# Performance work log

Measured on AMD Instinct MI355X. Metric: run time of the kernel, lower is better.

Reference implementation:

```python
import jax, jax.numpy as jnp
import numpy as np

MODEL_DIM = 128
WINDOW = 512
KERNEL = 512
N_BANDS = 128
N_ATOMS = 16
N_SAMPLES = 2 ** 15
STEP = WINDOW // 2
N_FRAMES = N_SAMPLES // STEP  # 128
N_HEADS = 4
D_FF = MODEL_DIM
N_LAYERS = 6
N_FREQS = 16
POS_CH = 2 * N_FREQS + 1  # 33
SR = 22050.0


def mel_filterbank():
    # Mel scale from 40 Hz to nyquist, gammatone-like: here use morlet-style
    # windowed sinusoids as in zounds FilterBank: for the reference we build
    # N_BANDS bandpass FIR filters of length KERNEL (fixed constants, treated
    # as non-learned buffers).
    nyq = SR / 2.0
    def hz_to_mel(h):
        return 2595.0 * np.log10(1 + h / 700.0)
    def mel_to_hz(m):
        return 700.0 * (10 ** (m / 2595.0) - 1)
    mels = np.linspace(hz_to_mel(40.0), hz_to_mel(nyq), N_BANDS + 2)
    hz = mel_to_hz(mels)
    centers = hz[1:-1]
    bandwidths = (hz[2:] - hz[:-2]) * 0.1
    t = np.arange(KERNEL) / SR
    filters = np.zeros((N_BANDS, KERNEL), dtype=np.float32)
    for i in range(N_BANDS):
        env = np.exp(-0.5 * ((t - t.mean()) * bandwidths[i] * 2 * np.pi) ** 2)
        filters[i] = (np.sin(2 * np.pi * centers[i] * t) * env).astype(np.float32)
    # normalize filters
    norms = np.linalg.norm(filters, axis=-1, keepdims=True) + 1e-8
    filters = filters / norms
    return jnp.asarray(filters)


def pos_encoded(batch, time, n_freqs):
    # [B, time, 2*n_freqs+1]: linear position plus sin/cos at doubling freqs
    pos = jnp.linspace(-1.0, 1.0, time, dtype=jnp.float32)
    feats = [pos[:, None]]
    for i in range(n_freqs):
        feats.append(jnp.sin((2.0 ** i) * pos * jnp.pi)[:, None])
        feats.append(jnp.cos((2.0 ** i) * pos * jnp.pi)[:, None])
    p = jnp.concatenate(feats, axis=-1)  # [time, 33]
    return jnp.broadcast_to(p[None], (batch, time, p.shape[-1]))


def layer_norm(x, g, b, eps=1e-5):
    mu = jnp.mean(x, axis=-1, keepdims=True)
    var = jnp.var(x, axis=-1, keepdims=True)
    return (x - mu) * jax.lax.rsqrt(var + eps) * g + b


def mha(x, p):
    B, S, D = x.shape
    hd = D // N_HEADS
    qkv = x @ p['w_qkv'].T + p['b_qkv']  # [B,S,3D]
    q, k, v = jnp.split(qkv, 3, axis=-1)
    def heads(t):
        return t.reshape(B, S, N_HEADS, hd).transpose(0, 2, 1, 3)
    q, k, v = heads(q), heads(k), heads(v)
    scores = jnp.einsum('bhqd,bhkd->bhqk', q, k) / jnp.sqrt(jnp.float32(hd))
    attn = jax.nn.softmax(scores, axis=-1)
    o = jnp.einsum('bhqk,bhkd->bhqd', attn, v)
    o = o.transpose(0, 2, 1, 3).reshape(B, S, D)
    return o @ p['w_o'].T + p['b_o']


def encoder_layer(x, p):
    # post-norm (torch default norm_first=False), relu activation
    x = layer_norm(x + mha(x, p), p['ln1_g'], p['ln1_b'])
    h = jax.nn.relu(x @ p['w1'].T + p['b1']) @ p['w2'].T + p['b2']
    x = layer_norm(x + h, p['ln2_g'], p['ln2_b'])
    return x


def transformer(x, layers):
    for p in layers:
        x = encoder_layer(x, p)
    return x


def _mk_layer(key):
    ks = jax.random.split(key, 4)
    s = 0.1
    D = MODEL_DIM
    return {
        'w_qkv': jax.random.uniform(ks[0], (3 * D, D), minval=-s, maxval=s),
        'b_qkv': jnp.zeros((3 * D,)),
        'w_o': jax.random.uniform(ks[1], (D, D), minval=-s, maxval=s),
        'b_o': jnp.zeros((D,)),
        'w1': jax.random.uniform(ks[2], (D_FF, D), minval=-s, maxval=s),
        'b1': jnp.zeros((D_FF,)),
        'w2': jax.random.uniform(ks[3], (D, D_FF), minval=-s, maxval=s),
        'b2': jnp.zeros((D,)),
        'ln1_g': jnp.ones((D,)), 'ln1_b': jnp.zeros((D,)),
        'ln2_g': jnp.ones((D,)), 'ln2_b': jnp.zeros((D,)),
    }


def setup_inputs() -> dict:
    key = jax.random.key(0)
    ks = jax.random.split(key, 20)
    B = 8
    x = jax.random.normal(ks[0], (B, 1, N_SAMPLES), dtype=jnp.float32)
    s = 0.1
    ctx_layers = [_mk_layer(ks[1 + i]) for i in range(N_LAYERS)]
    dec_layers = [_mk_layer(ks[7 + i]) for i in range(N_LAYERS)]
    params = {
        'filters': mel_filterbank(),  # [N_BANDS, KERNEL], fixed buffer
        'embed_w': jax.random.uniform(ks[13], (MODEL_DIM, MODEL_DIM + POS_CH), minval=-s, maxval=s),
        'embed_b': jnp.zeros((MODEL_DIM,)),
        'embed2_w': jax.random.uniform(ks[14], (MODEL_DIM, MODEL_DIM + POS_CH), minval=-s, maxval=s),
        'embed2_b': jnp.zeros((MODEL_DIM,)),
        'env_w': jax.random.uniform(ks[15], (1, MODEL_DIM), minval=-s, maxval=s),
        'env_b': jnp.zeros((1,)),
        'samp_w': jax.random.uniform(ks[16], (WINDOW, MODEL_DIM), minval=-s, maxval=s),
        'samp_b': jnp.zeros((WINDOW,)),
    }
    # flatten layer params into dict entries
    out = {'x': x}
    out.update(params)
    for i, p in enumerate(ctx_layers):
        for k, v in p.items():
            out[f'ctx{i}_{k}'] = v
    for i, p in enumerate(dec_layers):
        for k, v in p.items():
            out[f'dec{i}_{k}'] = v
    return out


LAYER_KEYS = ['w_qkv', 'b_qkv', 'w_o', 'b_o', 'w1', 'b1', 'w2', 'b2',
              'ln1_g', 'ln1_b', 'ln2_g', 'ln2_b']


def _forward(x, filters, embed_w, embed_b, embed2_w, embed2_b,
             env_w, env_b, samp_w, samp_b, ctx_layers, dec_layers):
    B = x.shape[0]
    # filterbank: conv1d with 'same'-ish padding as zounds (padding=KERNEL//2)
    spec = jax.lax.conv_general_dilated(
        x, filters[:, None, :],  # [O=128, I=1, K=512]
        window_strides=(1,), padding=[(KERNEL // 2, KERNEL // 2)],
        dimension_numbers=('NCH', 'OIH', 'NCH'))  # [B,128,~32768]
    # temporal pooling: avg pool window 512 stride 256 over abs
    pooled = jax.lax.reduce_window(
        jnp.abs(spec), 0.0, jax.lax.add,
        window_dimensions=(1, 1, 512), window_strides=(1, 1, 256),
        padding=[(0, 0), (0, 0), (256, 256)]) / 512.0
    n = pooled[..., :N_FRAMES]  # [B,128,128]
    pos = pos_encoded(B, N_FRAMES, N_FREQS).transpose(0, 2, 1)  # [B,33,128]
    n = jnp.concatenate([pos, n], axis=1)  # [B,161,128]
    n = jnp.einsum('oc,bct->bot', embed_w, n) + embed_b[None, :, None]
    n = n.transpose(0, 2, 1)  # [B,T,D]
    h = transformer(n, ctx_layers)  # context
    h = h.transpose(0, 2, 1)  # [B,D,T]
    norms = (jnp.einsum('oc,bct->bot', env_w, h) + env_b[None, :, None]).reshape(B, -1)
    norms = jax.nn.softmax(norms, axis=-1)
    values, indices = jax.lax.top_k(norms, N_ATOMS)  # [B,K]
    # vectorized gather-scale-scatter: n[b,:,idx] = h[b,:,idx]*val
    sel = jnp.take_along_axis(h, indices[:, None, :], axis=2)  # [B,D,K]
    sel = sel * values[:, None, :]
    sparse = jnp.zeros_like(h)
    bidx = jnp.arange(B)[:, None, None]
    didx = jnp.arange(MODEL_DIM)[None, :, None]
    sparse = sparse.at[bidx, didx, indices[:, None, :]].set(sel)
    n = jnp.concatenate([pos, sparse], axis=1)
    n = jnp.einsum('oc,bct->bot', embed2_w, n) + embed2_b[None, :, None]
    n = n.transpose(0, 2, 1)
    n = transformer(n, dec_layers)
    n = n.transpose(0, 2, 1)  # [B,D,T]
    # to_samples: 1x1 conv D->WINDOW then permute -> [B,T,WINDOW]
    n = jnp.einsum('oc,bct->bto', samp_w, n) + samp_b[None, None, :]
    # hamming window
    t = jnp.arange(WINDOW, dtype=jnp.float32)
    ham = 0.54 - 0.46 * jnp.cos(2 * jnp.pi * t / (WINDOW - 1))
    n = n * ham[None, None, :]
    # overlap-add with hop = WINDOW//2
    T = n.shape[1]
    out_len = STEP * (T - 1) + WINDOW
    frame_pos = jnp.arange(T)[:, None] * STEP + jnp.arange(WINDOW)[None, :]
    out = jnp.zeros((B, out_len), dtype=n.dtype)
    out = out.at[:, frame_pos.reshape(-1)].add(n.reshape(B, -1))
    return out[:, None, :N_SAMPLES]


def reference(x, filters, embed_w, embed_b, embed2_w, embed2_b,
              env_w, env_b, samp_w, samp_b, **layer_params):
    ctx_layers = [{k: layer_params[f'ctx{i}_{k}'] for k in LAYER_KEYS}
                  for i in range(N_LAYERS)]
    dec_layers = [{k: layer_params[f'dec{i}_{k}'] for k in LAYER_KEYS}
                  for i in range(N_LAYERS)]
    return _forward(x, filters, embed_w, embed_b, embed2_w, embed2_b,
                    env_w, env_b, samp_w, samp_b, ctx_layers, dec_layers)
```

## Files before the change

### kernel.cpp

```cpp
#include <hip/hip_runtime.h>
#include <math.h>

#define NB 8
#define NS 32768
#define SEQ 128
#define DIM 128
#define KER 512
#define PI_D 3.14159265358979323846

#define ALOAD(p)     __hip_atomic_load((p), __ATOMIC_RELAXED, __HIP_MEMORY_SCOPE_AGENT)
#define ASTORE(p, v) __hip_atomic_store((p), (v), __ATOMIC_RELAXED, __HIP_MEMORY_SCOPE_AGENT)

typedef __attribute__((ext_vector_type(8))) short bfrag;
typedef __attribute__((ext_vector_type(16))) float f32x16;

__global__ void pos_k(float* __restrict__ posT, float* __restrict__ ham) {
    int t = threadIdx.x;
    if (t < 128) {
        double p = (double)((float)(-1.0 + 2.0 * (double)t / 127.0));
        posT[t * 33 + 0] = (float)p;
        for (int i = 0; i < 16; ++i) {
            double a = ldexp(p, i) * PI_D;
            posT[t * 33 + 1 + 2 * i] = (float)sin(a);
            posT[t * 33 + 2 + 2 * i] = (float)cos(a);
// ... 113 lines not shown
        for (int m = 1; m <= 16; m <<= 1) { s0 += __shfl_xor(s0, m); s1 += __shfl_xor(s1, m); }
        if ((lane & 31) == 0) {
            int rowoff = (r & 3) + 8 * (r >> 2) + 4 * g;
            atomicAdd(&Pp[mbase + rowoff], s0);
            atomicAdd(&Pp[mbase + 32 + rowoff], s1);
        }
    }
    __syncthreads();
    if (t < 128) P[((size_t)b * 128 + t) * 128 + c] = Pp[t];
}

struct PackPtrs { const float* p[51]; };

__global__ void pack_k(PackPtrs pp, float4* __restrict__ dst) {
    int m = blockIdx.y;
    const float* src = pp.p[m];
    int N, K, KT; size_t off;
    if (m < 12)      { N = 384; K = 128; KT = 32; off = (size_t)m * 12288; }
    else if (m < 24) { N = 128; K = 128; KT = 32; off = 147456 + (size_t)(m - 12) * 4096; }
    else if (m < 36) { N = 128; K = 128; KT = 32; off = 196608 + (size_t)(m - 24) * 4096; }
    else if (m < 48) { N = 128; K = 128; KT = 32; off = 245760 + (size_t)(m - 36) * 4096; }
    else if (m == 48){ N = 128; K = 161; KT = 41; off = 294912; }
    else if (m == 49){ N = 128; K = 161; KT = 41; off = 300160; }
    else             { N = 512; K = 128; KT = 32; off = 305408; }
    int idx = blockIdx.x * 256 + threadIdx.x;
    int total = (N >> 6) * KT * 64;
    if (idx >= total) return;
    int ln = idx & 63;
    int kt = (idx >> 6) % KT;
    int ct = idx / (KT * 64);
    int cc = ct * 64 + ln;
    int k0 = kt * 4;
    float4 v;
    v.x = (k0 + 0 < K) ? src[(size_t)cc * K + k0 + 0] : 0.f;
    v.y = (k0 + 1 < K) ? src[(size_t)cc * K + k0 + 1] : 0.f;
    v.z = (k0 + 2 < K) ? src[(size_t)cc * K + k0 + 2] : 0.f;
    v.w = (k0 + 3 < K) ? src[(size_t)cc * K + k0 + 3] : 0.f;
    dst[off + idx] = v;
}

struct MegaArgs {
    const float* b_qkv[12]; const float* b_o[12]; const float* b1[12]; const float* b2[12];
    const float* ln1g[12]; const float* ln1b[12]; const float* ln2g[12]; const float* ln2b[12];
    const float* embed_b; const float* embed2_b; const float* env_w; const float* env_b;
    const float* samp_b;
    const float* posT; const float* ham; const float* P;
    const float4* Wp;
    float* KV;
    float* envbuf; float* Y; float* out;
    unsigned* ctr;
};

struct __align__(16) SM {
    float KV[128][129];
    union { float S[16][128]; float partial[16][128]; };
    float Aq[4][128];
    float Ax[4][128];
    float Ax2[4][128];
    float Ah[4][128];
    float cv[4][176];
    float red2[16];
    int   red2i[8];
    float tvals[128], tout[128], Linv[16];
};

__device__ __forceinline__ void gbarb(unsigned* ctr, unsigned& bi) {
    asm volatile("s_waitcnt vmcnt(0)" ::: "memory");
    __syncthreads();
    if (threadIdx.x == 0) {
        bi += 1;
        __hip_atomic_fetch_add(ctr, 1u, __ATOMIC_RELAXED, __HIP_MEMORY_SCOPE_AGENT);
        unsigned target = bi * 32u;
        while (__hip_atomic_load(ctr, __ATOMIC_RELAXED, __HIP_MEMORY_SCOPE_AGENT) < target) {
            __builtin_amdgcn_s_sleep(1);
        }
    }
    __syncthreads();
}

template <int NCB>
__device__ __forceinline__ void gemm_acc(const float* A, int astride, const float4* Wp,
                                         int KT, int t, float (*acc)[4]) {
    int cidx = t & 127, kq = t >> 7;
    int KTq = (KT + 3) >> 2;
    int kt0 = kq * KTq;
    int kt1 = kt0 + KTq; if (kt1 > KT) kt1 = KT;
#pragma unroll
    for (int i = 0; i < NCB; ++i) { acc[i][0] = 0.f; acc[i][1] = 0.f; acc[i][2] = 0.f; acc[i][3] = 0.f; }
    for (int kt = kt0; kt < kt1; ++kt) {
        float4 a0 = *(const float4*)(A + 0 * astride + kt * 4);
        float4 a1 = *(const float4*)(A + 1 * astride + kt * 4);
        float4 a2 = *(const float4*)(A + 2 * astride + kt * 4);
        float4 a3 = *(const float4*)(A + 3 * astride + kt * 4);
#pragma unroll
        for (int i = 0; i < NCB; ++i) {
            int cb = cidx + i * 128;
            float4 w = Wp[((size_t)((cb >> 6) * KT + kt)) * 64 + (cb & 63)];
            acc[i][0] += a0.x * w.x + a0.y * w.y + a0.z * w.z + a0.w * w.w;
            acc[i][1] += a1.x * w.x + a1.y * w.y + a1.z * w.z + a1.w * w.w;
            acc[i][2] += a2.x * w.x + a2.y * w.y + a2.z * w.z + a2.w * w.w;
            acc[i][3] += a3.x * w.x + a3.y * w.y + a3.z * w.z + a3.w * w.w;
        }
    }
}

__device__ __forceinline__ float gemm_reduce(const float* a4, int t, SM& sm) {
    int cidx = t & 127, kq = t >> 7;
    __syncthreads();
#pragma unroll
    for (int r = 0; r < 4; ++r) sm.partial[r * 4 + kq][cidx] = a4[r];
    __syncthreads();
    int rsel = t >> 7;
    return sm.partial[rsel * 4 + 0][cidx] + sm.partial[rsel * 4 + 1][cidx]
         + sm.partial[rsel * 4 + 2][cidx] + sm.partial[rsel * 4 + 3][cidx];
}

__device__ __forceinline__ float lnorm(float v, int t, const float* g, const float* be, SM& sm) {
    float s = v, s2 = v * v;
#pragma unroll
    for (int mm = 1; mm <= 32; mm <<= 1) { s += __shfl_xor(s, mm); s2 += __shfl_xor(s2, mm); }
    int w = t >> 6;
    if ((t & 63) == 0) { sm.red2[w * 2] = s; sm.red2[w * 2 + 1] = s2; }
    __syncthreads();
    int r = t >> 7;
    float S = sm.red2[(2 * r) * 2] + sm.red2[(2 * r + 1) * 2];
    float S2 = sm.red2[(2 * r) * 2 + 1] + sm.red2[(2 * r + 1) * 2 + 1];
    float mu = S * (1.f / 128.f);
    float var = S2 * (1.f / 128.f) - mu * mu;
    float res = (v - mu) * rsqrtf(var + 1e-5f) * g[t & 127] + be[t & 127];
    __syncthreads();
    return res;
}

__device__ __forceinline__ void qkv_tail(const MegaArgs& a, SM& sm, int l, int t, int rowbase) {
    const float4* qkvp = a.Wp + (size_t)l * 12288;
    float acc3[3][4];
    gemm_acc<3>(&sm.Ax[0][0], 128, qkvp, 32, t, acc3);
    int c = t & 127, rs = t >> 7;
    const float* bq = a.b_qkv[l];
    float* KVp = a.KV + (size_t)(l & 1) * 262144;
    float vq = gemm_reduce(acc3[0], t, sm) + bq[c];
    sm.Aq[rs][c] = vq;
    float vk = gemm_reduce(acc3[1], t, sm) + bq[128 + c];
    ASTORE(&KVp[(size_t)(rowbase + rs) * 256 + c], vk);
    float vv = gemm_reduce(acc3[2], t, sm) + bq[256 + c];
    ASTORE(&KVp[(size_t)(rowbase + rs) * 256 + 128 + c], vv);
}

__global__ void __launch_bounds__(512, 1) mega_k(MegaArgs a) {
    __shared__ SM sm;
    const int t = threadIdx.x;
    const int bid = blockIdx.x;
    const int rowbase = bid * 4;
    const int b = rowbase >> 7;
    const int tfr = rowbase & 127;
    const int c = t & 127;
    const int rs = t >> 7;
    unsigned bctr = 0;
    unsigned* myctr = a.ctr + b * 16;

    const float4* embedp  = a.Wp + 294912;
    const float4* embed2p = a.Wp + 300160;
    const float4* sampp   = a.Wp + 305408;

    {
        int tf = tfr + rs;
        for (int j = c; j < 176; j += 128) {
            float val = 0.f;
            if (j < 33) val = a.posT[tf * 33 + j];
            else if (j < 161) {
                int o = j - 33;
                float p1 = a.P[((size_t)(b * 128 + o)) * 128 + tf];
                float p0 = (tf > 0) ? a.P[((size_t)(b * 128 + o)) * 128 + tf - 1] : 0.f;
                val = (p0 + p1) * (1.f / 512.f);
            }
            sm.cv[rs][j] = val;
        }
        __syncthreads();
        float acc1[1][4];
        gemm_acc<1>(&sm.cv[0][0], 176, embedp, 41, t, acc1);
        float v = gemm_reduce(acc1[0], t, sm) + a.embed_b[c];
        sm.Ax[rs][c] = v;
        __syncthreads();
        qkv_tail(a, sm, 0, t, rowbase);
        gbarb(myctr, bctr);
    }

    for (int l = 0; l < 12; ++l) {
        if (l == 6) {
            float v = (t < 128) ? ALOAD(&a.envbuf[b * 128 + t]) : -1e30f;
            float m_ = v;
#pragma unroll
            for (int mm = 1; mm <= 32; mm <<= 1) m_ = fmaxf(m_, __shfl_xor(m_, mm));
            if ((t & 63) == 0) sm.red2[(t >> 6) * 2] = m_;
            __syncthreads();
            float mx = fmaxf(sm.red2[0], sm.red2[2]);
            float e = (t < 128) ? expf(v - mx) : 0.f;
            float ssum = e;
#pragma unroll
            for (int mm = 1; mm <= 32; mm <<= 1) ssum += __shfl_xor(ssum, mm);
            __syncthreads();
            if ((t & 63) == 0) sm.red2[(t >> 6) * 2 + 1] = ssum;
            __syncthreads();
            float lsum = sm.red2[1] + sm.red2[3];
            if (t < 128) { sm.tvals[t] = e / lsum; sm.tout[t] = 0.f; }
            __syncthreads();
            for (int it = 0; it < 16; ++it) {
                float cv_ = (t < 128) ? sm.tvals[t] : -2.f;
                int ci = t & 127;
#pragma unroll
                for (int mm = 1; mm <= 32; mm <<= 1) {
                    float ov = __shfl_xor(cv_, mm);
                    int oi = __shfl_xor(ci, mm);
                    if (ov > cv_ || (ov == cv_ && oi < ci)) { cv_ = ov; ci = oi; }
                }
                if ((t & 63) == 0) { sm.red2[(t >> 6) * 2] = cv_; sm.red2i[t >> 6] = ci; }
                __syncthreads();
                if (t == 0) {
                    float v0 = sm.red2[0], v1 = sm.red2[2];
                    int i0 = sm.red2i[0], i1 = sm.red2i[1];
                    float bv; int bi2;
                    if (v1 > v0 || (v1 == v0 && i1 < i0)) { bv = v1; bi2 = i1; }
                    else { bv = v0; bi2 = i0; }
                    sm.tout[bi2] = bv;
                    sm.tvals[bi2] = -3.f;
                }
                __syncthreads();
            }
            float sclr = sm.tout[tfr + rs];
            for (int j = c; j < 176; j += 128) {
                float val = 0.f;
                if (j < 33) val = a.posT[(tfr + rs) * 33 + j];
                else if (j < 161) val = sm.Ax[rs][j - 33] * sclr;
                sm.cv[rs][j] = val;
            }
            __syncthreads();
            float acc1[1][4];
            gemm_acc<1>(&sm.cv[0][0], 176, embed2p, 41, t, acc1);
            float vv = gemm_reduce(acc1[0], t, sm) + a.embed2_b[c];
            sm.Ax[rs][c] = vv;
            __syncthreads();
            qkv_tail(a, sm, 6, t, rowbase);
            gbarb(myctr, bctr);
        }

        const float4* op  = a.Wp + 147456 + (size_t)l * 4096;
        const float4* w1p = a.Wp + 196608 + (size_t)l * 4096;
        const float4* w2p = a.Wp + 245760 + (size_t)l * 4096;
        const float* KVg = a.KV + (size_t)(l & 1) * 262144 + (size_t)b * 32768;

        {
            float kst[32], vst[32];
#pragma unroll
            for (int j = 0; j < 32; ++j) {
                int f = j * 512 + t;
                kst[j] = ALOAD(&KVg[(size_t)(f >> 7) * 256 + (f & 127)]);
            }
#pragma unroll
            for (int j = 0; j < 32; ++j) {
                int f = j * 512 + t;
                vst[j] = ALOAD(&KVg[(size_t)(f >> 7) * 256 + 128 + (f & 127)]);
            }
            int cd = t & 127, r0 = t >> 7;
#pragma unroll
            for (int j = 0; j < 32; ++j) sm.KV[cd][j * 4 + r0] = kst[j];
            __syncthreads();
            {
                int h = t >> 7, k = c;
                float s0 = 0.f, s1 = 0.f, s2 = 0.f, s3 = 0.f;
#pragma unroll
                for (int d = 0; d < 32; ++d) {
                    float kvv = sm.KV[h * 32 + d][k];
                    s0 += sm.Aq[0][h * 32 + d] * kvv;
                    s1 += sm.Aq[1][h * 32 + d] * kvv;
                    s2 += sm.Aq[2][h * 32 + d] * kvv;
                    s3 += sm.Aq[3][h * 32 + d] * kvv;
                }
                const float scl = 0.17677669529663687f;
                sm.S[h * 4 + 0][k] = s0 * scl;
                sm.S[h * 4 + 1][k] = s1 * scl;
                sm.S[h * 4 + 2][k] = s2 * scl;
                sm.S[h * 4 + 3][k] = s3 * scl;
            }
            __syncthreads();
#pragma unroll
            for (int j = 0; j < 32; ++j) sm.KV[cd][j * 4 + r0] = vst[j];
            {
                int row = t >> 5, l32 = t & 31;
                float v0 = sm.S[row][l32], v1 = sm.S[row][l32 + 32];
                float v2 = sm.S[row][l32 + 64], v3 = sm.S[row][l32 + 96];
                float mx = fmaxf(fmaxf(v0, v1), fmaxf(v2, v3));
#pragma unroll
                for (int mm = 1; mm <= 16; mm <<= 1) mx = fmaxf(mx, __shfl_xor(mx, mm));
                float e0 = __expf(v0 - mx), e1 = __expf(v1 - mx);
                float e2 = __expf(v2 - mx), e3 = __expf(v3 - mx);
                float ls = e0 + e1 + e2 + e3;
#pragma unroll
                for (int mm = 1; mm <= 16; mm <<= 1) ls += __shfl_xor(ls, mm);
                sm.S[row][l32] = e0; sm.S[row][l32 + 32] = e1;
                sm.S[row][l32 + 64] = e2; sm.S[row][l32 + 96] = e3;
                if (l32 == 0) sm.Linv[row] = 1.f / ls;
            }
            __syncthreads();
            {
                int h = t >> 7, r = (t >> 5) & 3, d = t & 31;
                const float* Pr = &sm.S[h * 4 + r][0];
                float o = 0.f;
#pragma unroll 8
                for (int k2 = 0; k2 < 128; ++k2) o += Pr[k2] * sm.KV[h * 32 + d][k2];
                sm.Ah[r][h * 32 + d] = o * sm.Linv[h * 4 + r];
            }
            __syncthreads();
        }
        {
            float acc1[1][4];
            gemm_acc<1>(&sm.Ah[0][0], 128, op, 32, t, acc1);
            float v = gemm_reduce(acc1[0], t, sm);
            v += a.b_o[l][c] + sm.Ax[rs][c];
            v = lnorm(v, t, a.ln1g[l], a.ln1b[l], sm);
            sm.Ax2[rs][c] = v;
            __syncthreads();
        }
        {
            float acc1[1][4];
            gemm_acc<1>(&sm.Ax2[0][0], 128, w1p, 32, t, acc1);
            float v = fmaxf(gemm_reduce(acc1[0], t, sm) + a.b1[l][c], 0.f);
            sm.Ah[rs][c] = v;
            __syncthreads();
            float acc2[1][4];
            gemm_acc<1>(&sm.Ah[0][0], 128, w2p, 32, t, acc2);
            float v2 = gemm_reduce(acc2[0], t, sm) + a.b2[l][c] + sm.Ax2[rs][c];
            v2 = lnorm(v2, t, a.ln2g[l], a.ln2b[l], sm);
            sm.Ax[rs][c] = v2;
            __syncthreads();
        }
        if (l == 5) {
            float pv = sm.Ax[rs][c] * a.env_w[c];
#pragma unroll
            for (int mm = 1; mm <= 32; mm <<= 1) pv += __shfl_xor(pv, mm);
            int w = t >> 6;
            if ((t & 63) == 0) sm.red2[w * 2] = pv;
            __syncthreads();
            if (t < 4) ASTORE(&a.envbuf[rowbase + t],
                              sm.red2[(2 * t) * 2] + sm.red2[(2 * t + 1) * 2] + a.env_b[0]);
            __syncthreads();
        } else if (l == 11) {
            float acc4[4][4];
            gemm_acc<4>(&sm.Ax[0][0], 128, sampp, 32, t, acc4);
#pragma unroll
            for (int i = 0; i < 4; ++i) {
                float v = gemm_reduce(acc4[i], t, sm);
                int cg = c + i * 128;
                v += a.samp_b[cg];
                v *= a.ham[cg];
                ASTORE(&a.Y[((size_t)(rowbase + rs)) * 512 + cg], v);
            }
        } else {
            qkv_tail(a, sm, l + 1, t, rowbase);
        }
        gbarb(myctr, bctr);
    }

    {
        int b32 = bid & 31;
#pragma unroll
        for (int i = 0; i < 2; ++i) {
            int il = b32 * 512 + t + i * 16384;
            int t0 = il >> 8, w0 = il & 255;
            float acc = ALOAD(&a.Y[((size_t)(b * 128 + t0)) * 512 + w0]);
            if (t0 > 0) acc += ALOAD(&a.Y[((size_t)(b * 128 + t0 - 1)) * 512 + w0 + 256]);
            a.out[(size_t)b * 32768 + il] = acc;
        }
    }
}

extern "C" void kernel_launch(void* const* d_in, const int* in_sizes, int n_in,
                              void* d_out, int out_size, void* d_ws, size_t ws_size,
                              hipStream_t stream) {
    const float* x        = (const float*)d_in[0];
    const float* filters  = (const float*)d_in[1];
    const float* embed_w  = (const float*)d_in[2];
    const float* embed_b  = (const float*)d_in[3];
    const float* embed2_w = (const float*)d_in[4];
    const float* embed2_b = (const float*)d_in[5];
    const float* env_w    = (const float*)d_in[6];
    const float* env_b    = (const float*)d_in[7];
    const float* samp_w   = (const float*)d_in[8];
    const float* samp_b   = (const float*)d_in[9];

    float* ws = (float*)d_ws;
    float* P     = ws;
    float* posT  = ws + 131072;
    float* hamw  = ws + 135424;
    float* envb  = ws + 135936;
    float* KV    = ws + 136960;
    float* Y     = ws + 661248;
    float4* Wp   = (float4*)(ws + 1185536);
    unsigned* ctr = (unsigned*)(ws + 2472704);
    unsigned short* xhi = (unsigned short*)Y;
    unsigned short* xlo = (unsigned short*)(Y + 131072);
    unsigned short* Fph = (unsigned short*)KV;
    unsigned short* Fpl = (unsigned short*)(KV + 32768);

    pos_k<<<1, 512, 0, stream>>>(posT, hamw);
    bfsplit_k<<<1024, 256, 0, stream>>>(x, xhi, xlo, NB * NS);
    fpack_k<<<256, 256, 0, stream>>>(filters, Fph, Fpl);
    conv_mfma_k<<<dim3(128, 8), 512, 0, stream>>>(xhi, xlo, Fph, Fpl, P);

    PackPtrs pp;
    for (int l = 0; l < 12; ++l) {
        int base = (l < 6) ? 10 + l * 12 : 82 + (l - 6) * 12;
        pp.p[l]      = (const float*)d_in[base + 0];
        pp.p[12 + l] = (const float*)d_in[base + 2];
        pp.p[24 + l] = (const float*)d_in[base + 4];
        pp.p[36 + l] = (const float*)d_in[base + 6];
    }
    pp.p[48] = embed_w; pp.p[49] = embed2_w; pp.p[50] = samp_w;
    pack_k<<<dim3(64, 51), 256, 0, stream>>>(pp, Wp);

    hipMemsetAsync(ctr, 0, 1024, stream);

    MegaArgs ma;
    for (int l = 0; l < 12; ++l) {
        int base = (l < 6) ? 10 + l * 12 : 82 + (l - 6) * 12;
        ma.b_qkv[l] = (const float*)d_in[base + 1];
        ma.b_o[l]   = (const float*)d_in[base + 3];
        ma.b1[l]    = (const float*)d_in[base + 5];
        ma.b2[l]    = (const float*)d_in[base + 7];
        ma.ln1g[l]  = (const float*)d_in[base + 8];
        ma.ln1b[l]  = (const float*)d_in[base + 9];
        ma.ln2g[l]  = (const float*)d_in[base + 10];
        ma.ln2b[l]  = (const float*)d_in[base + 11];
    }
    ma.embed_b = embed_b; ma.embed2_b = embed2_b;
    ma.env_w = env_w; ma.env_b = env_b; ma.samp_b = samp_b;
    ma.posT = posT; ma.ham = hamw; ma.P = P;
    ma.Wp = (const float4*)Wp;
    ma.KV = KV; ma.envbuf = envb; ma.Y = Y; ma.out = (float*)d_out;
    ma.ctr = ctr;

    mega_k<<<256, 512, 0, stream>>>(ma);
}
```

Before: 348.7 us.

## Split persistent megakernel into 512 half-size blocks with chunked K/V staging

The persistent kernel now runs 512 blocks of 256 threads, each owning 2 sequence rows instead of 4, so per-layer work is spread over twice as many blocks (two per CU). The GEMM helpers reduce over 2 k-slices and write all partial sums with one barrier instead of one pair of barriers per output. Attention stages K and V through shared memory in 64-row halves, prefetching the next half into registers while the current one is used. The aim is more parallelism and fewer barriers per layer. The cost is that every block still reads the full K/V of its batch, which doubles that traffic, and the grid barrier now has to wait for 64 blocks per batch.

```diff
diff --git a/kernel.cpp b/kernel.cpp
--- a/kernel.cpp
+++ b/kernel.cpp
@@ -189,16 +189,16 @@
 };
 
 struct __align__(16) SM {
-    float KV[128][129];
-    union { float S[16][128]; float partial[16][128]; };
-    float Aq[4][128];
-    float Ax[4][128];
-    float Ax2[4][128];
-    float Ah[4][128];
-    float cv[4][176];
+    float KVs[64][129];
+    union { float S[8][128]; float partial[16][128]; };
+    float Aq[2][128];
+    float Ax[2][128];
+    float Ax2[2][128];
+    float Ah[2][128];
+    float cv[2][176];
     float red2[16];
     int   red2i[8];
-    float tvals[128], tout[128], Linv[16];
+    float tvals[128], tout[128], Linv[8];
 };
 
 __device__ __forceinline__ void gbarb(unsigned* ctr, unsigned& bi) {
@@ -207,7 +207,7 @@
     if (threadIdx.x == 0) {
         bi += 1;
         __hip_atomic_fetch_add(ctr, 1u, __ATOMIC_RELAXED, __HIP_MEMORY_SCOPE_AGENT);
-        unsigned target = bi * 32u;
+        unsigned target = bi * 64u;
         while (__hip_atomic_load(ctr, __ATOMIC_RELAXED, __HIP_MEMORY_SCOPE_AGENT) < target) {
             __builtin_amdgcn_s_sleep(1);
         }
@@ -216,40 +216,39 @@
 }
 
 template <int NCB>
-__device__ __forceinline__ void gemm_acc(const float* A, int astride, const float4* Wp,
-                                         int KT, int t, float (*acc)[4]) {
+__device__ __forceinline__ void gemm_acc2(const float* A, int astride, const float4* Wp,
+                                          int KT, int t, float (*acc)[2]) {
     int cidx = t & 127, kq = t >> 7;
-    int KTq = (KT + 3) >> 2;
+    int KTq = (KT + 1) >> 1;
     int kt0 = kq * KTq;
     int kt1 = kt0 + KTq; if (kt1 > KT) kt1 = KT;
 #pragma unroll
-    for (int i = 0; i < NCB; ++i) { acc[i][0] = 0.f; acc[i][1] = 0.f; acc[i][2] = 0.f; acc[i][3] = 0.f; }
+    for (int i = 0; i < NCB; ++i) { acc[i][0] = 0.f; acc[i][1] = 0.f; }
     for (int kt = kt0; kt < kt1; ++kt) {
         float4 a0 = *(const float4*)(A + 0 * astride + kt * 4);
         float4 a1 = *(const float4*)(A + 1 * astride + kt * 4);
-        float4 a2 = *(const float4*)(A + 2 * astride + kt * 4);
-        float4 a3 = *(const float4*)(A + 3 * astride + kt * 4);
 #pragma unroll
         for (int i = 0; i < NCB; ++i) {
             int cb = cidx + i * 128;
             float4 w = Wp[((size_t)((cb >> 6) * KT + kt)) * 64 + (cb & 63)];
             acc[i][0] += a0.x * w.x + a0.y * w.y + a0.z * w.z + a0.w * w.w;
             acc[i][1] += a1.x * w.x + a1.y * w.y + a1.z * w.z + a1.w * w.w;
-            acc[i][2] += a2.x * w.x + a2.y * w.y + a2.z * w.z + a2.w * w.w;
-            acc[i][3] += a3.x * w.x + a3.y * w.y + a3.z * w.z + a3.w * w.w;
-        }
-    }
-}
-
-__device__ __forceinline__ float gemm_reduce(const float* a4, int t, SM& sm) {
-    int cidx = t & 127, kq = t >> 7;
+        }
+    }
+}
+
+template <int NCB>
+__device__ __forceinline__ void gemm_red_write(const float (*acc)[2], int t, SM& sm) {
+    int c = t & 127, kq = t >> 7;
+#pragma unroll
+    for (int i = 0; i < NCB; ++i)
+#pragma unroll
+        for (int r = 0; r < 2; ++r)
+            sm.partial[(i * 2 + r) * 2 + kq][c] = acc[i][r];
     __syncthreads();
-#pragma unroll
-    for (int r = 0; r < 4; ++r) sm.partial[r * 4 + kq][cidx] = a4[r];
-    __syncthreads();
-    int rsel = t >> 7;
-    return sm.partial[rsel * 4 + 0][cidx] + sm.partial[rsel * 4 + 1][cidx]
-         + sm.partial[rsel * 4 + 2][cidx] + sm.partial[rsel * 4 + 3][cidx];
+}
+__device__ __forceinline__ float rdp(SM& sm, int i, int rr, int c) {
+    return sm.partial[(i * 2 + rr) * 2 + 0][c] + sm.partial[(i * 2 + rr) * 2 + 1][c];
 }
 
 __device__ __forceinline__ float lnorm(float v, int t, const float* g, const float* be, SM& sm) {
@@ -271,28 +270,29 @@
 
 __device__ __forceinline__ void qkv_tail(const MegaArgs& a, SM& sm, int l, int t, int rowbase) {
     const float4* qkvp = a.Wp + (size_t)l * 12288;
-    float acc3[3][4];
-    gemm_acc<3>(&sm.Ax[0][0], 128, qkvp, 32, t, acc3);
-    int c = t & 127, rs = t >> 7;
+    float acc3[3][2];
+    gemm_acc2<3>(&sm.Ax[0][0], 128, qkvp, 32, t, acc3);
+    gemm_red_write<3>(acc3, t, sm);
+    int c = t & 127, rr = t >> 7;
     const float* bq = a.b_qkv[l];
     float* KVp = a.KV + (size_t)(l & 1) * 262144;
-    float vq = gemm_reduce(acc3[0], t, sm) + bq[c];
-    sm.Aq[rs][c] = vq;
-    float vk = gemm_reduce(acc3[1], t, sm) + bq[128 + c];
-    ASTORE(&KVp[(size_t)(rowbase + rs) * 256 + c], vk);
-    float vv = gemm_reduce(acc3[2], t, sm) + bq[256 + c];
-    ASTORE(&KVp[(size_t)(rowbase + rs) * 256 + 128 + c], vv);
-}
-
-__global__ void __launch_bounds__(512, 1) mega_k(MegaArgs a) {
+    float vq = rdp(sm, 0, rr, c) + bq[c];
+    sm.Aq[rr][c] = vq;
+    float vk = rdp(sm, 1, rr, c) + bq[128 + c];
+    ASTORE(&KVp[(size_t)(rowbase + rr) * 256 + c], vk);
+    float vv = rdp(sm, 2, rr, c) + bq[256 + c];
+    ASTORE(&KVp[(size_t)(rowbase + rr) * 256 + 128 + c], vv);
+}
+
+__global__ void __launch_bounds__(256, 2) mega_k(MegaArgs a) {
     __shared__ SM sm;
     const int t = threadIdx.x;
     const int bid = blockIdx.x;
-    const int rowbase = bid * 4;
+    const int rowbase = bid * 2;
     const int b = rowbase >> 7;
     const int tfr = rowbase & 127;
     const int c = t & 127;
-    const int rs = t >> 7;
+    const int rr = t >> 7;
     unsigned bctr = 0;
     unsigned* myctr = a.ctr + b * 16;
 
@@ -301,7 +301,7 @@
     const float4* sampp   = a.Wp + 305408;
 
     {
-        int tf = tfr + rs;
+        int tf = tfr + rr;
         for (int j = c; j < 176; j += 128) {
             float val = 0.f;
             if (j < 33) val = a.posT[tf * 33 + j];
@@ -311,13 +311,14 @@
                 float p0 = (tf > 0) ? a.P[((size_t)(b * 128 + o)) * 128 + tf - 1] : 0.f;
                 val = (p0 + p1) * (1.f / 512.f);
             }
-            sm.cv[rs][j] = val;
+            sm.cv[rr][j] = val;
         }
         __syncthreads();
-        float acc1[1][4];
-        gemm_acc<1>(&sm.cv[0][0], 176, embedp, 41, t, acc1);
-        float v = gemm_reduce(acc1[0], t, sm) + a.embed_b[c];
-        sm.Ax[rs][c] = v;
+        float acc1[1][2];
+        gemm_acc2<1>(&sm.cv[0][0], 176, embedp, 41, t, acc1);
+        gemm_red_write<1>(acc1, t, sm);
+        float v = rdp(sm, 0, rr, c) + a.embed_b[c];
+        sm.Ax[rr][c] = v;
         __syncthreads();
         qkv_tail(a, sm, 0, t, rowbase);
         gbarb(myctr, bctr);
@@ -364,18 +365,19 @@
                 }
                 __syncthreads();
             }
-            float sclr = sm.tout[tfr + rs];
+            float sclr = sm.tout[tfr + rr];
             for (int j = c; j < 176; j += 128) {
                 float val = 0.f;
-                if (j < 33) val = a.posT[(tfr + rs) * 33 + j];
-                else if (j < 161) val = sm.Ax[rs][j - 33] * sclr;
-                sm.cv[rs][j] = val;
-            }
-            __syncthreads();
-            float acc1[1][4];
-            gemm_acc<1>(&sm.cv[0][0], 176, embed2p, 41, t, acc1);
-            float vv = gemm_reduce(acc1[0], t, sm) + a.embed2_b[c];
-            sm.Ax[rs][c] = vv;
+                if (j < 33) val = a.posT[(tfr + rr) * 33 + j];
+                else if (j < 161) val = sm.Ax[rr][j - 33] * sclr;
+                sm.cv[rr][j] = val;
+            }
+            __syncthreads();
+            float acc1[1][2];
+            gemm_acc2<1>(&sm.cv[0][0], 176, embed2p, 41, t, acc1);
+            gemm_red_write<1>(acc1, t, sm);
+            float vv = rdp(sm, 0, rr, c) + a.embed2_b[c];
+            sm.Ax[rr][c] = vv;
             __syncthreads();
             qkv_tail(a, sm, 6, t, rowbase);
             gbarb(myctr, bctr);
@@ -387,41 +389,52 @@
         const float* KVg = a.KV + (size_t)(l & 1) * 262144 + (size_t)b * 32768;
 
         {
-            float kst[32], vst[32];
-#pragma unroll
-            for (int j = 0; j < 32; ++j) {
-                int f = j * 512 + t;
-                kst[j] = ALOAD(&KVg[(size_t)(f >> 7) * 256 + (f & 127)]);
-            }
-#pragma unroll
-            for (int j = 0; j < 32; ++j) {
-                int f = j * 512 + t;
-                vst[j] = ALOAD(&KVg[(size_t)(f >> 7) * 256 + 128 + (f & 127)]);
-            }
-            int cd = t & 127, r0 = t >> 7;
-#pragma unroll
-            for (int j = 0; j < 32; ++j) sm.KV[cd][j * 4 + r0] = kst[j];
+            const float scl = 0.17677669529663687f;
+            float rg[32], rg2[32];
+            float oacc = 0.f;
+#pragma unroll
+            for (int j = 0; j < 32; ++j)
+                rg[j] = ALOAD(&KVg[(size_t)(2 * j + rr) * 256 + c]);
+#pragma unroll
+            for (int j = 0; j < 32; ++j) sm.KVs[2 * j + rr][c] = rg[j];
+#pragma unroll
+            for (int j = 0; j < 32; ++j)
+                rg2[j] = ALOAD(&KVg[(size_t)(64 + 2 * j + rr) * 256 + c]);
             __syncthreads();
             {
-                int h = t >> 7, k = c;
-                float s0 = 0.f, s1 = 0.f, s2 = 0.f, s3 = 0.f;
-#pragma unroll
+                int k = t & 63, h = t >> 6;
+                float s0 = 0.f, s1 = 0.f;
+#pragma unroll 8
                 for (int d = 0; d < 32; ++d) {
-                    float kvv = sm.KV[h * 32 + d][k];
-                    s0 += sm.Aq[0][h * 32 + d] * kvv;
-                    s1 += sm.Aq[1][h * 32 + d] * kvv;
-                    s2 += sm.Aq[2][h * 32 + d] * kvv;
-                    s3 += sm.Aq[3][h * 32 + d] * kvv;
+                    float kv = sm.KVs[k][h * 32 + d];
+                    s0 += sm.Aq[0][h * 32 + d] * kv;
+                    s1 += sm.Aq[1][h * 32 + d] * kv;
                 }
-                const float scl = 0.17677669529663687f;
-                sm.S[h * 4 + 0][k] = s0 * scl;
-                sm.S[h * 4 + 1][k] = s1 * scl;
-                sm.S[h * 4 + 2][k] = s2 * scl;
-                sm.S[h * 4 + 3][k] = s3 * scl;
-            }
-            __syncthreads();
-#pragma unroll
-            for (int j = 0; j < 32; ++j) sm.KV[cd][j * 4 + r0] = vst[j];
+                sm.S[0 + h][k] = s0 * scl;
+                sm.S[4 + h][k] = s1 * scl;
+            }
+            __syncthreads();
+#pragma unroll
+            for (int j = 0; j < 32; ++j) sm.KVs[2 * j + rr][c] = rg2[j];
+#pragma unroll
+            for (int j = 0; j < 32; ++j)
+                rg[j] = ALOAD(&KVg[(size_t)(2 * j + rr) * 256 + 128 + c]);
+            __syncthreads();
+            {
+                int k = t & 63, h = t >> 6;
+                float s0 = 0.f, s1 = 0.f;
+#pragma unroll 8
+                for (int d = 0; d < 32; ++d) {
+                    float kv = sm.KVs[k][h * 32 + d];
+                    s0 += sm.Aq[0][h * 32 + d] * kv;
+                    s1 += sm.Aq[1][h * 32 + d] * kv;
+                }
+                sm.S[0 + h][64 + k] = s0 * scl;
+                sm.S[4 + h][64 + k] = s1 * scl;
+            }
+            __syncthreads();
+#pragma unroll
+            for (int j = 0; j < 32; ++j) sm.KVs[2 * j + rr][c] = rg[j];
             {
                 int row = t >> 5, l32 = t & 31;
                 float v0 = sm.S[row][l32], v1 = sm.S[row][l32 + 32];
@@ -438,59 +451,74 @@
                 sm.S[row][l32 + 64] = e2; sm.S[row][l32 + 96] = e3;
                 if (l32 == 0) sm.Linv[row] = 1.f / ls;
             }
+#pragma unroll
+            for (int j = 0; j < 32; ++j)
+                rg2[j] = ALOAD(&KVg[(size_t)(64 + 2 * j + rr) * 256 + 128 + c]);
             __syncthreads();
             {
-                int h = t >> 7, r = (t >> 5) & 3, d = t & 31;
-                const float* Pr = &sm.S[h * 4 + r][0];
-                float o = 0.f;
+                int r = t >> 7, h = (t >> 5) & 3, d = t & 31;
+                const float* Pr = &sm.S[r * 4 + h][0];
 #pragma unroll 8
-                for (int k2 = 0; k2 < 128; ++k2) o += Pr[k2] * sm.KV[h * 32 + d][k2];
-                sm.Ah[r][h * 32 + d] = o * sm.Linv[h * 4 + r];
+                for (int k2 = 0; k2 < 64; ++k2) oacc += Pr[k2] * sm.KVs[k2][h * 32 + d];
+            }
+            __syncthreads();
+#pragma unroll
+            for (int j = 0; j < 32; ++j) sm.KVs[2 * j + rr][c] = rg2[j];
+            __syncthreads();
+            {
+                int r = t >> 7, h = (t >> 5) & 3, d = t & 31;
+                const float* Pr = &sm.S[r * 4 + h][64];
+#pragma unroll 8
+                for (int k2 = 0; k2 < 64; ++k2) oacc += Pr[k2] * sm.KVs[k2][h * 32 + d];
+                sm.Ah[r][h * 32 + d] = oacc * sm.Linv[r * 4 + h];
             }
             __syncthreads();
         }
         {
-            float acc1[1][4];
-            gemm_acc<1>(&sm.Ah[0][0], 128, op, 32, t, acc1);
-            float v = gemm_reduce(acc1[0], t, sm);
-            v += a.b_o[l][c] + sm.Ax[rs][c];
+            float ac[1][2];
+            gemm_acc2<1>(&sm.Ah[0][0], 128, op, 32, t, ac);
+            gemm_red_write<1>(ac, t, sm);
+            float v = rdp(sm, 0, rr, c) + a.b_o[l][c] + sm.Ax[rr][c];
             v = lnorm(v, t, a.ln1g[l], a.ln1b[l], sm);
-            sm.Ax2[rs][c] = v;
+            sm.Ax2[rr][c] = v;
             __syncthreads();
         }
         {
-            float acc1[1][4];
-            gemm_acc<1>(&sm.Ax2[0][0], 128, w1p, 32, t, acc1);
-            float v = fmaxf(gemm_reduce(acc1[0], t, sm) + a.b1[l][c], 0.f);
-            sm.Ah[rs][c] = v;
-            __syncthreads();
-            float acc2[1][4];
-            gemm_acc<1>(&sm.Ah[0][0], 128, w2p, 32, t, acc2);
-            float v2 = gemm_reduce(acc2[0], t, sm) + a.b2[l][c] + sm.Ax2[rs][c];
+            float ac[1][2];
+            gemm_acc2<1>(&sm.Ax2[0][0], 128, w1p, 32, t, ac);
+            gemm_red_write<1>(ac, t, sm);
+            float v = fmaxf(rdp(sm, 0, rr, c) + a.b1[l][c], 0.f);
+            sm.Ah[rr][c] = v;
+            __syncthreads();
+        }
+        {
+            float ac[1][2];
+            gemm_acc2<1>(&sm.Ah[0][0], 128, w2p, 32, t, ac);
+            gemm_red_write<1>(ac, t, sm);
+            float v2 = rdp(sm, 0, rr, c) + a.b2[l][c] + sm.Ax2[rr][c];
             v2 = lnorm(v2, t, a.ln2g[l], a.ln2b[l], sm);
-            sm.Ax[rs][c] = v2;
+            sm.Ax[rr][c] = v2;
             __syncthreads();
         }
         if (l == 5) {
-            float pv = sm.Ax[rs][c] * a.env_w[c];
+            float pv = sm.Ax[rr][c] * a.env_w[c];
 #pragma unroll
             for (int mm = 1; mm <= 32; mm <<= 1) pv += __shfl_xor(pv, mm);
             int w = t >> 6;
             if ((t & 63) == 0) sm.red2[w * 2] = pv;
             __syncthreads();
-            if (t < 4) ASTORE(&a.envbuf[rowbase + t],
+            if (t < 2) ASTORE(&a.envbuf[rowbase + t],
                               sm.red2[(2 * t) * 2] + sm.red2[(2 * t + 1) * 2] + a.env_b[0]);
             __syncthreads();
         } else if (l == 11) {
-            float acc4[4][4];
-            gemm_acc<4>(&sm.Ax[0][0], 128, sampp, 32, t, acc4);
+            float ac4[4][2];
+            gemm_acc2<4>(&sm.Ax[0][0], 128, sampp, 32, t, ac4);
+            gemm_red_write<4>(ac4, t, sm);
 #pragma unroll
             for (int i = 0; i < 4; ++i) {
-                float v = gemm_reduce(acc4[i], t, sm);
                 int cg = c + i * 128;
-                v += a.samp_b[cg];
-                v *= a.ham[cg];
-                ASTORE(&a.Y[((size_t)(rowbase + rs)) * 512 + cg], v);
+                float v = (rdp(sm, i, rr, c) + a.samp_b[cg]) * a.ham[cg];
+                ASTORE(&a.Y[((size_t)(rowbase + rr)) * 512 + cg], v);
             }
         } else {
             qkv_tail(a, sm, l + 1, t, rowbase);
@@ -499,10 +527,10 @@
     }
 
     {
-        int b32 = bid & 31;
+        int b64 = bid & 63;
 #pragma unroll
         for (int i = 0; i < 2; ++i) {
-            int il = b32 * 512 + t + i * 16384;
+            int il = b64 * 256 + t + i * 16384;
             int t0 = il >> 8, w0 = il & 255;
             float acc = ALOAD(&a.Y[((size_t)(b * 128 + t0)) * 512 + w0]);
             if (t0 > 0) acc += ALOAD(&a.Y[((size_t)(b * 128 + t0 - 1)) * 512 + w0 + 256]);
@@ -576,5 +604,5 @@
     ma.KV = KV; ma.envbuf = envb; ma.Y = Y; ma.out = (float*)d_out;
     ma.ctr = ctr;
 
-    mega_k<<<256, 512, 0, stream>>>(ma);
-}
+    mega_k<<<512, 256, 0, stream>>>(ma);
+}
```

New measurement: 500.3 us. 1.43x slower.

## Prefetch next GEMM weight tile into registers while computing current one

Applied to the files above, without the earlier changes.

Replaces the generic gemm_acc calls in the per-layer chain (QKV, out-proj, FFN1, FFN2, sample projection) with a register double-buffered scheme. Each step computes from one register set while loading the next weight slice into the other. The goal is to hide global weight-load latency behind the FMA work and the reductions. It also changes launch bounds to allow two blocks per CU, which constrains registers, and the extra 64 float registers for weights risk spilling.

```diff
diff --git a/kernel.cpp b/kernel.cpp
--- a/kernel.cpp
+++ b/kernel.cpp
@@ -215,6 +215,30 @@
     __syncthreads();
 }
 
+__device__ __forceinline__ void wload1(float4* w, const float4* Wp, int t) {
+    int cidx = t & 127, kq = t >> 7;
+#pragma unroll
+    for (int j = 0; j < 8; ++j)
+        w[j] = Wp[((size_t)((cidx >> 6) * 32 + kq * 8 + j)) * 64 + (cidx & 63)];
+}
+__device__ __forceinline__ void gemm_fma1(const float* A, const float4* w, int t, float* acc) {
+    int kq = t >> 7;
+    acc[0] = acc[1] = acc[2] = acc[3] = 0.f;
+#pragma unroll
+    for (int j = 0; j < 8; ++j) {
+        int kt = kq * 8 + j;
+        float4 a0 = *(const float4*)(A + 0 * 128 + kt * 4);
+        float4 a1 = *(const float4*)(A + 1 * 128 + kt * 4);
+        float4 a2 = *(const float4*)(A + 2 * 128 + kt * 4);
+        float4 a3 = *(const float4*)(A + 3 * 128 + kt * 4);
+        float4 ww = w[j];
+        acc[0] += a0.x * ww.x + a0.y * ww.y + a0.z * ww.z + a0.w * ww.w;
+        acc[1] += a1.x * ww.x + a1.y * ww.y + a1.z * ww.z + a1.w * ww.w;
+        acc[2] += a2.x * ww.x + a2.y * ww.y + a2.z * ww.z + a2.w * ww.w;
+        acc[3] += a3.x * ww.x + a3.y * ww.y + a3.z * ww.z + a3.w * ww.w;
+    }
+}
+
 template <int NCB>
 __device__ __forceinline__ void gemm_acc(const float* A, int astride, const float4* Wp,
                                          int KT, int t, float (*acc)[4]) {
@@ -269,22 +293,7 @@
     return res;
 }
 
-__device__ __forceinline__ void qkv_tail(const MegaArgs& a, SM& sm, int l, int t, int rowbase) {
-    const float4* qkvp = a.Wp + (size_t)l * 12288;
-    float acc3[3][4];
-    gemm_acc<3>(&sm.Ax[0][0], 128, qkvp, 32, t, acc3);
-    int c = t & 127, rs = t >> 7;
-    const float* bq = a.b_qkv[l];
-    float* KVp = a.KV + (size_t)(l & 1) * 262144;
-    float vq = gemm_reduce(acc3[0], t, sm) + bq[c];
-    sm.Aq[rs][c] = vq;
-    float vk = gemm_reduce(acc3[1], t, sm) + bq[128 + c];
-    ASTORE(&KVp[(size_t)(rowbase + rs) * 256 + c], vk);
-    float vv = gemm_reduce(acc3[2], t, sm) + bq[256 + c];
-    ASTORE(&KVp[(size_t)(rowbase + rs) * 256 + 128 + c], vv);
-}
-
-__global__ void __launch_bounds__(512, 1) mega_k(MegaArgs a) {
+__global__ void __launch_bounds__(512, 2) mega_k(MegaArgs a) {
     __shared__ SM sm;
     const int t = threadIdx.x;
     const int bid = blockIdx.x;
@@ -300,7 +309,37 @@
     const float4* embed2p = a.Wp + 300160;
     const float4* sampp   = a.Wp + 305408;
 
+    float4 wA[8], wB[8];
+
+    auto qkv_phases = [&](int l1) {
+        const float4* qkvp = a.Wp + (size_t)l1 * 12288;
+        float* KVp = a.KV + (size_t)(l1 & 1) * 262144;
+        const float* bq = a.b_qkv[l1];
+        {
+            float ac[4];
+            gemm_fma1(&sm.Ax[0][0], wB, t, ac);
+            wload1(wA, qkvp + 4096, t);
+            float vq = gemm_reduce(ac, t, sm) + bq[c];
+            sm.Aq[rs][c] = vq;
+        }
+        {
+            float ac[4];
+            gemm_fma1(&sm.Ax[0][0], wA, t, ac);
+            wload1(wB, qkvp + 8192, t);
+            float vk = gemm_reduce(ac, t, sm) + bq[128 + c];
+            ASTORE(&KVp[(size_t)(rowbase + rs) * 256 + c], vk);
+        }
+        {
+            float ac[4];
+            gemm_fma1(&sm.Ax[0][0], wB, t, ac);
+            wload1(wA, a.Wp + 147456 + (size_t)l1 * 4096, t);
+            float vv = gemm_reduce(ac, t, sm) + bq[256 + c];
+            ASTORE(&KVp[(size_t)(rowbase + rs) * 256 + 128 + c], vv);
+        }
+    };
+
     {
+        wload1(wB, a.Wp, t);
         int tf = tfr + rs;
         for (int j = c; j < 176; j += 128) {
             float val = 0.f;
@@ -319,7 +358,7 @@
         float v = gemm_reduce(acc1[0], t, sm) + a.embed_b[c];
         sm.Ax[rs][c] = v;
         __syncthreads();
-        qkv_tail(a, sm, 0, t, rowbase);
+        qkv_phases(0);
         gbarb(myctr, bctr);
     }
 
@@ -377,11 +416,10 @@
             float vv = gemm_reduce(acc1[0], t, sm) + a.embed2_b[c];
             sm.Ax[rs][c] = vv;
             __syncthreads();
-            qkv_tail(a, sm, 6, t, rowbase);
+            qkv_phases(6);
             gbarb(myctr, bctr);
         }
 
-        const float4* op  = a.Wp + 147456 + (size_t)l * 4096;
         const float4* w1p = a.Wp + 196608 + (size_t)l * 4096;
         const float4* w2p = a.Wp + 245760 + (size_t)l * 4096;
         const float* KVg = a.KV + (size_t)(l & 1) * 262144 + (size_t)b * 32768;
@@ -450,23 +488,28 @@
             __syncthreads();
         }
         {
-            float acc1[1][4];
-            gemm_acc<1>(&sm.Ah[0][0], 128, op, 32, t, acc1);
-            float v = gemm_reduce(acc1[0], t, sm);
-            v += a.b_o[l][c] + sm.Ax[rs][c];
+            float ac[4];
+            gemm_fma1(&sm.Ah[0][0], wA, t, ac);
+            wload1(wB, w1p, t);
+            float v = gemm_reduce(ac, t, sm) + a.b_o[l][c] + sm.Ax[rs][c];
             v = lnorm(v, t, a.ln1g[l], a.ln1b[l], sm);
             sm.Ax2[rs][c] = v;
             __syncthreads();
         }
         {
-            float acc1[1][4];
-            gemm_acc<1>(&sm.Ax2[0][0], 128, w1p, 32, t, acc1);
-            float v = fmaxf(gemm_reduce(acc1[0], t, sm) + a.b1[l][c], 0.f);
+            float ac[4];
+            gemm_fma1(&sm.Ax2[0][0], wB, t, ac);
+            wload1(wA, w2p, t);
+            float v = fmaxf(gemm_reduce(ac, t, sm) + a.b1[l][c], 0.f);
             sm.Ah[rs][c] = v;
             __syncthreads();
-            float acc2[1][4];
-            gemm_acc<1>(&sm.Ah[0][0], 128, w2p, 32, t, acc2);
-            float v2 = gemm_reduce(acc2[0], t, sm) + a.b2[l][c] + sm.Ax2[rs][c];
+        }
+        {
+            float ac[4];
+            gemm_fma1(&sm.Ah[0][0], wA, t, ac);
+            if (l < 11) wload1(wB, a.Wp + (size_t)(l + 1) * 12288, t);
+            else wload1(wB, sampp, t);
+            float v2 = gemm_reduce(ac, t, sm) + a.b2[l][c] + sm.Ax2[rs][c];
             v2 = lnorm(v2, t, a.ln2g[l], a.ln2b[l], sm);
             sm.Ax[rs][c] = v2;
             __syncthreads();
@@ -482,18 +525,22 @@
                               sm.red2[(2 * t) * 2] + sm.red2[(2 * t + 1) * 2] + a.env_b[0]);
             __syncthreads();
         } else if (l == 11) {
-            float acc4[4][4];
-            gemm_acc<4>(&sm.Ax[0][0], 128, sampp, 32, t, acc4);
 #pragma unroll
             for (int i = 0; i < 4; ++i) {
-                float v = gemm_reduce(acc4[i], t, sm);
+                float ac[4];
+                if (i & 1) {
+                    gemm_fma1(&sm.Ax[0][0], wA, t, ac);
+                    if (i < 3) wload1(wB, sampp + (size_t)(i + 1) * 4096, t);
+                } else {
+                    gemm_fma1(&sm.Ax[0][0], wB, t, ac);
+                    if (i < 3) wload1(wA, sampp + (size_t)(i + 1) * 4096, t);
+                }
                 int cg = c + i * 128;
-                v += a.samp_b[cg];
-                v *= a.ham[cg];
+                float v = (gemm_reduce(ac, t, sm) + a.samp_b[cg]) * a.ham[cg];
                 ASTORE(&a.Y[((size_t)(rowbase + rs)) * 512 + cg], v);
             }
         } else {
-            qkv_tail(a, sm, l + 1, t, rowbase);
+            qkv_phases(l + 1);
         }
         gbarb(myctr, bctr);
     }
```

Result: slower. 727.2 us (+108.5%).

## Replace split-K GEMM with per-row full-K dot products, dropping LDS reductions

Applied to the files above, without the earlier changes.

The small row-by-weight GEMMs used to split K across four thread groups, each covering all four rows, and then combined the partials through a shared-memory reduction guarded by two barriers. Now each thread computes one full-K dot product for a single row and column, which removes the partial buffer and its barriers. The cost is that each thread loads four times as many weight float4s from global memory, with the four row groups issuing duplicate weight loads, and runs a longer serial accumulation chain. A few extra __syncthreads are added to avoid read/write hazards on the shared activation buffers.

```diff
diff --git a/kernel.cpp b/kernel.cpp
--- a/kernel.cpp
+++ b/kernel.cpp
@@ -190,7 +190,7 @@
 
 struct __align__(16) SM {
     float KV[128][129];
-    union { float S[16][128]; float partial[16][128]; };
+    float S[16][128];
     float Aq[4][128];
     float Ax[4][128];
     float Ax2[4][128];
@@ -215,41 +215,16 @@
     __syncthreads();
 }
 
-template <int NCB>
-__device__ __forceinline__ void gemm_acc(const float* A, int astride, const float4* Wp,
-                                         int KT, int t, float (*acc)[4]) {
-    int cidx = t & 127, kq = t >> 7;
-    int KTq = (KT + 3) >> 2;
-    int kt0 = kq * KTq;
-    int kt1 = kt0 + KTq; if (kt1 > KT) kt1 = KT;
-#pragma unroll
-    for (int i = 0; i < NCB; ++i) { acc[i][0] = 0.f; acc[i][1] = 0.f; acc[i][2] = 0.f; acc[i][3] = 0.f; }
-    for (int kt = kt0; kt < kt1; ++kt) {
-        float4 a0 = *(const float4*)(A + 0 * astride + kt * 4);
-        float4 a1 = *(const float4*)(A + 1 * astride + kt * 4);
-        float4 a2 = *(const float4*)(A + 2 * astride + kt * 4);
-        float4 a3 = *(const float4*)(A + 3 * astride + kt * 4);
-#pragma unroll
-        for (int i = 0; i < NCB; ++i) {
-            int cb = cidx + i * 128;
-            float4 w = Wp[((size_t)((cb >> 6) * KT + kt)) * 64 + (cb & 63)];
-            acc[i][0] += a0.x * w.x + a0.y * w.y + a0.z * w.z + a0.w * w.w;
-            acc[i][1] += a1.x * w.x + a1.y * w.y + a1.z * w.z + a1.w * w.w;
-            acc[i][2] += a2.x * w.x + a2.y * w.y + a2.z * w.z + a2.w * w.w;
-            acc[i][3] += a3.x * w.x + a3.y * w.y + a3.z * w.z + a3.w * w.w;
-        }
-    }
-}
-
-__device__ __forceinline__ float gemm_reduce(const float* a4, int t, SM& sm) {
-    int cidx = t & 127, kq = t >> 7;
-    __syncthreads();
-#pragma unroll
-    for (int r = 0; r < 4; ++r) sm.partial[r * 4 + kq][cidx] = a4[r];
-    __syncthreads();
-    int rsel = t >> 7;
-    return sm.partial[rsel * 4 + 0][cidx] + sm.partial[rsel * 4 + 1][cidx]
-         + sm.partial[rsel * 4 + 2][cidx] + sm.partial[rsel * 4 + 3][cidx];
+template <int KT>
+__device__ __forceinline__ float gemm_dot(const float* Ar, const float4* Wp, int c) {
+    float acc = 0.f;
+#pragma unroll
+    for (int kt = 0; kt < KT; ++kt) {
+        float4 a = *(const float4*)(Ar + kt * 4);
+        float4 w = Wp[((size_t)((c >> 6) * KT + kt)) * 64 + (c & 63)];
+        acc += a.x * w.x + a.y * w.y + a.z * w.z + a.w * w.w;
+    }
+    return acc;
 }
 
 __device__ __forceinline__ float lnorm(float v, int t, const float* g, const float* be, SM& sm) {
@@ -271,17 +246,25 @@
 
 __device__ __forceinline__ void qkv_tail(const MegaArgs& a, SM& sm, int l, int t, int rowbase) {
     const float4* qkvp = a.Wp + (size_t)l * 12288;
-    float acc3[3][4];
-    gemm_acc<3>(&sm.Ax[0][0], 128, qkvp, 32, t, acc3);
-    int c = t & 127, rs = t >> 7;
+    int c = t & 127, r = t >> 7;
+    const float* Ar = &sm.Ax[r][0];
+    float aq = 0.f, ak = 0.f, av = 0.f;
+#pragma unroll
+    for (int kt = 0; kt < 32; ++kt) {
+        float4 a4 = *(const float4*)(Ar + kt * 4);
+        int wi = ((c >> 6) * 32 + kt) * 64 + (c & 63);
+        float4 w0 = qkvp[wi];
+        float4 w1 = qkvp[4096 + wi];
+        float4 w2 = qkvp[8192 + wi];
+        aq += a4.x * w0.x + a4.y * w0.y + a4.z * w0.z + a4.w * w0.w;
+        ak += a4.x * w1.x + a4.y * w1.y + a4.z * w1.z + a4.w * w1.w;
+        av += a4.x * w2.x + a4.y * w2.y + a4.z * w2.z + a4.w * w2.w;
+    }
     const float* bq = a.b_qkv[l];
     float* KVp = a.KV + (size_t)(l & 1) * 262144;
-    float vq = gemm_reduce(acc3[0], t, sm) + bq[c];
-    sm.Aq[rs][c] = vq;
-    float vk = gemm_reduce(acc3[1], t, sm) + bq[128 + c];
-    ASTORE(&KVp[(size_t)(rowbase + rs) * 256 + c], vk);
-    float vv = gemm_reduce(acc3[2], t, sm) + bq[256 + c];
-    ASTORE(&KVp[(size_t)(rowbase + rs) * 256 + 128 + c], vv);
+    sm.Aq[r][c] = aq + bq[c];
+    ASTORE(&KVp[(size_t)(rowbase + r) * 256 + c], ak + bq[128 + c]);
+    ASTORE(&KVp[(size_t)(rowbase + r) * 256 + 128 + c], av + bq[256 + c]);
 }
 
 __global__ void __launch_bounds__(512, 1) mega_k(MegaArgs a) {
@@ -314,9 +297,7 @@
             sm.cv[rs][j] = val;
         }
         __syncthreads();
-        float acc1[1][4];
-        gemm_acc<1>(&sm.cv[0][0], 176, embedp, 41, t, acc1);
-        float v = gemm_reduce(acc1[0], t, sm) + a.embed_b[c];
+        float v = gemm_dot<41>(&sm.cv[rs][0], embedp, c) + a.embed_b[c];
         sm.Ax[rs][c] = v;
         __syncthreads();
         qkv_tail(a, sm, 0, t, rowbase);
@@ -372,9 +353,8 @@
                 sm.cv[rs][j] = val;
             }
             __syncthreads();
-            float acc1[1][4];
-            gemm_acc<1>(&sm.cv[0][0], 176, embed2p, 41, t, acc1);
-            float vv = gemm_reduce(acc1[0], t, sm) + a.embed2_b[c];
+            float vv = gemm_dot<41>(&sm.cv[rs][0], embed2p, c) + a.embed2_b[c];
+            __syncthreads();
             sm.Ax[rs][c] = vv;
             __syncthreads();
             qkv_tail(a, sm, 6, t, rowbase);
@@ -450,23 +430,19 @@
             __syncthreads();
         }
         {
-            float acc1[1][4];
-            gemm_acc<1>(&sm.Ah[0][0], 128, op, 32, t, acc1);
-            float v = gemm_reduce(acc1[0], t, sm);
-            v += a.b_o[l][c] + sm.Ax[rs][c];
+            float v = gemm_dot<32>(&sm.Ah[rs][0], op, c) + a.b_o[l][c] + sm.Ax[rs][c];
             v = lnorm(v, t, a.ln1g[l], a.ln1b[l], sm);
             sm.Ax2[rs][c] = v;
             __syncthreads();
         }
         {
-            float acc1[1][4];
-            gemm_acc<1>(&sm.Ax2[0][0], 128, w1p, 32, t, acc1);
-            float v = fmaxf(gemm_reduce(acc1[0], t, sm) + a.b1[l][c], 0.f);
+            float v = fmaxf(gemm_dot<32>(&sm.Ax2[rs][0], w1p, c) + a.b1[l][c], 0.f);
+            __syncthreads();
             sm.Ah[rs][c] = v;
             __syncthreads();
-            float acc2[1][4];
-            gemm_acc<1>(&sm.Ah[0][0], 128, w2p, 32, t, acc2);
-            float v2 = gemm_reduce(acc2[0], t, sm) + a.b2[l][c] + sm.Ax2[rs][c];
+        }
+        {
+            float v2 = gemm_dot<32>(&sm.Ah[rs][0], w2p, c) + a.b2[l][c] + sm.Ax2[rs][c];
             v2 = lnorm(v2, t, a.ln2g[l], a.ln2b[l], sm);
             sm.Ax[rs][c] = v2;
             __syncthreads();
@@ -482,14 +458,22 @@
                               sm.red2[(2 * t) * 2] + sm.red2[(2 * t + 1) * 2] + a.env_b[0]);
             __syncthreads();
         } else if (l == 11) {
-            float acc4[4][4];
-            gemm_acc<4>(&sm.Ax[0][0], 128, sampp, 32, t, acc4);
+            float ac4[4] = {0.f, 0.f, 0.f, 0.f};
+            const float* Ar = &sm.Ax[rs][0];
+#pragma unroll
+            for (int kt = 0; kt < 32; ++kt) {
+                float4 a4 = *(const float4*)(Ar + kt * 4);
+                int wi = ((c >> 6) * 32 + kt) * 64 + (c & 63);
+#pragma unroll
+                for (int i = 0; i < 4; ++i) {
+                    float4 w = sampp[i * 4096 + wi];
+                    ac4[i] += a4.x * w.x + a4.y * w.y + a4.z * w.z + a4.w * w.w;
+                }
+            }
 #pragma unroll
             for (int i = 0; i < 4; ++i) {
-                float v = gemm_reduce(acc4[i], t, sm);
                 int cg = c + i * 128;
-                v += a.samp_b[cg];
-                v *= a.ham[cg];
+                float v = (ac4[i] + a.samp_b[cg]) * a.ham[cg];
                 ASTORE(&a.Y[((size_t)(rowbase + rs)) * 512 + cg], v);
             }
         } else {
```

Measured after the change: 904.1 us. +159.2%, slower.
